# Kernel tuning notes

Measured on AMD Instinct MI355X. Metric: run time of the kernel, lower is better.

The kernel has to match this reference:

```python
import jax, jax.numpy as jnp
import numpy as np

# dims
N, T, DIN = 256, 32, 2048      # batch, time, gpt output dim
H = 2048                        # MLP hidden
G, C, D = 2, 16, 256            # vq groups, codebook size, code dim
W, A = 5, 7                     # action window, action dim
WA = W * A                      # output_size
DEC_H = 512                     # vqvae decoder hidden
NT = N * T


def _mk(key, shape, scale=0.02):
    return jax.random.normal(key, shape, dtype=jnp.float32) * scale


def setup_inputs() -> dict:
    key = jax.random.key(0)
    ks = jax.random.split(key, 16)
    inp = {
        "x": jax.random.normal(ks[0], (N, T, DIN), dtype=jnp.float32),
        # bin1 MLP: DIN -> H -> H -> C
        "w11": _mk(ks[1], (DIN, H)), "b11": jnp.zeros((H,), jnp.float32),
        "w12": _mk(ks[2], (H, H)),   "b12": jnp.zeros((H,), jnp.float32),
        "w13": _mk(ks[3], (H, C)),   "b13": jnp.zeros((C,), jnp.float32),
        # bin2 MLP: DIN+C -> H -> C
        "w21": _mk(ks[4], (DIN + C, H)), "b21": jnp.zeros((H,), jnp.float32),
        "w22": _mk(ks[5], (H, C)),       "b22": jnp.zeros((C,), jnp.float32),
        # offset MLP: DIN -> H -> H -> G*C*WA
        "wo1": _mk(ks[6], (DIN, H)), "bo1": jnp.zeros((H,), jnp.float32),
        "wo2": _mk(ks[7], (H, H)),   "bo2": jnp.zeros((H,), jnp.float32),
        "wo3": _mk(ks[8], (H, G * C * WA)), "bo3": jnp.zeros((G * C * WA,), jnp.float32),
        # residual-VQ codebooks: (G, C, D)
        "codebook": _mk(ks[9], (G, C, D), scale=1.0),
        # frozen vqvae decoder: G*D -> DEC_H -> WA
        "wd1": _mk(ks[10], (G * D, DEC_H)), "bd1": jnp.zeros((DEC_H,), jnp.float32),
        "wd2": _mk(ks[11], (DEC_H, WA)),    "bd2": jnp.zeros((WA,), jnp.float32),
    }
    return inp


def reference(x, w11, b11, w12, b12, w13, b13, w21, b21, w22, b22,
              wo1, bo1, wo2, bo2, wo3, bo3, codebook, wd1, bd1, wd2, bd2):
    xf = x.reshape(NT, DIN)
    # bin1 logits
    h = jax.nn.relu(xf @ w11 + b11)
    h = jax.nn.relu(h @ w12 + b12)
    cbet_logits1 = h @ w13 + b13                       # (NT, C)
    # offsets
    o = jax.nn.relu(xf @ wo1 + bo1)
    o = jax.nn.relu(o @ wo2 + bo2)
    cbet_offsets = (o @ wo3 + bo3).reshape(NT, G, C, WA)
    # multinomial sampling (== categorical over softmax(logits))
    key = jax.random.key(42)
    k1, k2 = jax.random.split(key)
    s1 = jax.random.categorical(k1, cbet_logits1)      # (NT,)
    one_hot1 = jax.nn.one_hot(s1, C, dtype=xf.dtype)
    h2 = jax.nn.relu(jnp.concatenate([xf, one_hot1], axis=1) @ w21 + b21)
    cbet_logits2 = h2 @ w22 + b22                      # (NT, C)
    s2 = jax.random.categorical(k2, cbet_logits2)
    sampled_centers = jnp.stack([s1, s2], axis=1)      # (NT, G)
    # gather offsets at sampled codes, sum over groups
    nt_idx = jnp.arange(NT)[:, None]
    g_idx = jnp.arange(G)[None, :]
    sampled_offsets = cbet_offsets[nt_idx, g_idx, sampled_centers].sum(axis=1)  # (NT, WA)
    # vq codebook lookup + frozen decoder (detached in torch)
    centers = codebook[g_idx, sampled_centers]          # (NT, G, D)
    dec_in = jax.lax.stop_gradient(centers.reshape(NT, G * D))
    decoded = jax.nn.relu(dec_in @ wd1 + bd1) @ wd2 + bd2
    decoded = jax.lax.stop_gradient(decoded)            # (NT, WA)
    predicted = (decoded.reshape(NT, W, A) + sampled_offsets.reshape(NT, W, A))
    predicted_action = predicted.reshape(N, T, WA)
    return predicted_action, decoded, cbet_logits1, cbet_logits2, sampled_centers
```

## Files before the change

### kernel.cpp

```cpp
#include <hip/hip_runtime.h>
#include <cstdint>
#include <cstddef>

#define NT_   8192
#define DIN_  2048
#define H_    2048
#define C_    16
#define G_    2
#define D_    256
#define WA_   35
#define DECH_ 512
#define NPAD_ 1152

typedef _Float16 f16;
typedef _Float16 h4 __attribute__((ext_vector_type(4)));
typedef _Float16 h8 __attribute__((ext_vector_type(8)));
typedef float fx4 __attribute__((ext_vector_type(4)));

typedef __attribute__((address_space(1))) const void gvoid_t;
typedef __attribute__((address_space(3))) void lvoid_t;

__device__ __forceinline__ void gld16(const void* g, void* l) {
  __builtin_amdgcn_global_load_lds((gvoid_t*)(uintptr_t)g,
                                   (lvoid_t*)(uint32_t)(uintptr_t)l, 16, 0, 0);
}

__device__ __forceinline__ void barrier_() {
  asm volatile("" ::: "memory");
  __builtin_amdgcn_s_barrier();
  asm volatile("" ::: "memory");
}

#define MFMA_(d, a, b) d = __builtin_amdgcn_mfma_f32_16x16x32_f16(a, b, d, 0, 0, 0)

__host__ __device__ inline void tf2x32(uint32_t k0, uint32_t k1,
                                       uint32_t x0, uint32_t x1,
                                       uint32_t& o0, uint32_t& o1) {
  const uint32_t ks2 = k0 ^ k1 ^ 0x1BD11BDAu;
  uint32_t ks[3] = {k0, k1, ks2};
  x0 += ks[0]; x1 += ks[1];
  const uint32_t R0[4] = {13u, 15u, 26u, 6u};
  const uint32_t R1[4] = {17u, 29u, 16u, 24u};
#pragma unroll
  for (int g = 0; g < 5; ++g) {
    const uint32_t* R = (g & 1) ? R1 : R0;
#pragma unroll
    for (int r = 0; r < 4; ++r) {
      x0 += x1;
      x1 = (x1 << R[r]) | (x1 >> (32u - R[r]));
      x1 ^= x0;
    }
    x0 += ks[(g + 1) % 3];
    x1 += ks[(g + 2) % 3] + (uint32_t)(g + 1);
  }
  o0 = x0; o1 = x1;
}

__global__ __launch_bounds__(256) void xsplit_kernel(
    const float* __restrict__ x, f16* __restrict__ xh, f16* __restrict__ xl) {
  const size_t i = (size_t)blockIdx.x * 256 + threadIdx.x;
  const float4 v0 = *(const float4*)(x + i * 8);
  const float4 v1 = *(const float4*)(x + i * 8 + 4);
  float vv[8] = {v0.x, v0.y, v0.z, v0.w, v1.x, v1.y, v1.z, v1.w};
  h8 hh, ll;
#pragma unroll
  for (int k = 0; k < 8; ++k) {
    const f16 h = (f16)vv[k];
    hh[k] = h;
    ll[k] = (f16)(vv[k] - (float)h);
  }
  *(h8*)(xh + i * 8) = hh;
  *(h8*)(xl + i * 8) = ll;
}

enum { EPI_PAIR = 0, EPI_HI = 1, EPI_LOGIT = 2 };

template <int TERMS, int GATHER, int EPI>
__global__ __launch_bounds__(512, 2) void gemm256(
    const f16* __restrict__ Ah, const f16* __restrict__ Al,
    const f16* __restrict__ Bh, const f16* __restrict__ Bl,
    const float* __restrict__ bias,
    f16* __restrict__ Chi, f16* __restrict__ Clo,
    int M, int N, int K,
    const int* __restrict__ gidx, const float* __restrict__ growp, int gldw,
    const float* __restrict__ wlog, float* __restrict__ part) {
  extern __shared__ f16 lds[];
  constexpr int BS = ((TERMS == 3) ? 4 : 2) * 8192;
  constexpr int NGLD = (TERMS == 3) ? 8 : 4;

  const int tid  = threadIdx.x;
  const int wave = tid >> 6;
  const int lane = tid & 63;
  const int lr   = lane & 15;

  const int nb  = N >> 8;
  const int nwg = (int)gridDim.x;
  const int qq  = nwg >> 3;
  const int sw  = ((int)blockIdx.x & 7) * qq + ((int)blockIdx.x >> 3);
  const int by  = sw / nb, bx = sw % nb;
  const int m0  = by << 8, n0 = bx << 8;

  const int wm = (wave >> 2) * 128;
  const int wn = (wave & 3) * 64;

  fx4 acc[8][4];
#pragma unroll
  for (int i = 0; i < 8; ++i)
#pragma unroll
    for (int j = 0; j < 4; ++j) acc[i][j] = (fx4){0.f, 0.f, 0.f, 0.f};

  const int r_row = wave * 16 + (lane >> 2);
  const int r_g   = (lane & 3) ^ ((lane >> 3) & 3);
  const f16* gsrc[NGLD];
  int gdst[NGLD];
  {
    int nr = 0;
    auto AR = [&](const f16* P, int mn, int reg, int rb) {
      gsrc[nr] = P + (size_t)(mn + rb + r_row) * K + r_g * 8;
      gdst[nr] = reg * 8192 + rb * 32 + wave * 512;
      ++nr;
    };
    if constexpr (TERMS == 3) {
      AR(Ah, m0, 0, 0); AR(Ah, m0, 0, 128);
      AR(Al, m0, 1, 0); AR(Al, m0, 1, 128);
      AR(Bh, n0, 2, 0); AR(Bh, n0, 2, 128);
      AR(Bl, n0, 3, 0); AR(Bl, n0, 3, 128);
    } else {
      AR(Ah, m0, 0, 0); AR(Ah, m0, 0, 128);
      AR(Bh, n0, 1, 0); AR(Bh, n0, 1, 128);
    }
  }

#pragma unroll
  for (int r = 0; r < NGLD; ++r) gld16(gsrc[r], lds + gdst[r]);
  asm volatile("s_waitcnt vmcnt(0)" ::: "memory");
  barrier_();

  const int pg8 = ((lane >> 4) ^ ((lr >> 1) & 3)) * 8;
  const int KT  = K >> 5;

  for (int t = 0; t < KT; ++t) {
    f16* const sb  = lds + (t & 1) * BS;
    f16* const nsb = lds + ((t + 1) & 1) * BS;
    const int ktn = (t + 1 < KT ? t + 1 : t) * 32;

    const f16* sAh = sb;
    const f16* sAl = sb + 8192;
    const f16* sBh = sb + (TERMS == 3 ? 2 : 1) * 8192;
    const f16* sBl = sb + 3 * 8192;

    h8 vbh[4], vbl[4], va[4];
#pragma unroll
    for (int j = 0; j < 4; ++j) {
      vbh[j] = *(const h8*)(sBh + (wn + j * 16 + lr) * 32 + pg8);
      if constexpr (TERMS == 3)
        vbl[j] = *(const h8*)(sBl + (wn + j * 16 + lr) * 32 + pg8);
    }
#pragma unroll
    for (int i = 0; i < 4; ++i)
      va[i] = *(const h8*)(sAh + (wm + i * 16 + lr) * 32 + pg8);
    gld16(gsrc[0] + ktn, nsb + gdst[0]);
    gld16(gsrc[1] + ktn, nsb + gdst[1]);
    if constexpr (TERMS == 3) gld16(gsrc[2] + ktn, nsb + gdst[2]);
    barrier_();
    asm volatile("s_waitcnt lgkmcnt(0)" ::: "memory");
    __builtin_amdgcn_sched_barrier(0);
    __builtin_amdgcn_s_setprio(1);
#pragma unroll
    for (int i = 0; i < 4; ++i)
#pragma unroll
      for (int j = 0; j < 4; ++j) MFMA_(acc[i][j], va[i], vbh[j]);
    if constexpr (TERMS == 3) {
#pragma unroll
      for (int i = 0; i < 4; ++i)
#pragma unroll
        for (int j = 0; j < 4; ++j) MFMA_(acc[i][j], va[i], vbl[j]);
    }
    __builtin_amdgcn_s_setprio(0);
    barrier_();
#pragma unroll
    for (int i = 0; i < 4; ++i)
      va[i] = *(const h8*)(sAh + (wm + 64 + i * 16 + lr) * 32 + pg8);
    if constexpr (TERMS == 3) {
      gld16(gsrc[3] + ktn, nsb + gdst[3]);
      gld16(gsrc[4] + ktn, nsb + gdst[4]);
      gld16(gsrc[5] + ktn, nsb + gdst[5]);
    } else {
      gld16(gsrc[2] + ktn, nsb + gdst[2]);
      gld16(gsrc[3] + ktn, nsb + gdst[3]);
    }
    barrier_();
    asm volatile("s_waitcnt lgkmcnt(0)" ::: "memory");
    __builtin_amdgcn_sched_barrier(0);
    __builtin_amdgcn_s_setprio(1);
#pragma unroll
    for (int i = 0; i < 4; ++i)
#pragma unroll
      for (int j = 0; j < 4; ++j) MFMA_(acc[4 + i][j], va[i], vbh[j]);
    if constexpr (TERMS == 3) {
#pragma unroll
      for (int i = 0; i < 4; ++i)
#pragma unroll
        for (int j = 0; j < 4; ++j) MFMA_(acc[4 + i][j], va[i], vbl[j]);
    }
    __builtin_amdgcn_s_setprio(0);
    if constexpr (TERMS != 3) asm volatile("s_waitcnt vmcnt(0)" ::: "memory");
    barrier_();
    if constexpr (TERMS == 3) {
      h8 vl0[4], vl1[4];
#pragma unroll
      for (int i = 0; i < 4; ++i) {
        vl0[i] = *(const h8*)(sAl + (wm + i * 16 + lr) * 32 + pg8);
        vl1[i] = *(const h8*)(sAl + (wm + 64 + i * 16 + lr) * 32 + pg8);
      }
      gld16(gsrc[6] + ktn, nsb + gdst[6]);
      gld16(gsrc[7] + ktn, nsb + gdst[7]);
      barrier_();
      asm volatile("s_waitcnt lgkmcnt(0)" ::: "memory");
      __builtin_amdgcn_sched_barrier(0);
      __builtin_amdgcn_s_setprio(1);
#pragma unroll
      for (int i = 0; i < 4; ++i)
#pragma unroll
        for (int j = 0; j < 4; ++j) {
          MFMA_(acc[i][j], vl0[i], vbh[j]);
          MFMA_(acc[4 + i][j], vl1[i], vbh[j]);
        }
      __builtin_amdgcn_s_setprio(0);
      asm volatile("s_waitcnt vmcnt(0)" ::: "memory");
      barrier_();
    }
  }

  const int rq = (lane >> 4) * 4;
  if constexpr (EPI == EPI_LOGIT) {
#pragma unroll
    for (int mi = 0; mi < 8; ++mi) {
#pragma unroll
      for (int q = 0; q < 4; ++q) {
        const int row = m0 + wm + mi * 16 + rq + q;
        const float* gr = nullptr;
        if constexpr (GATHER) gr = growp + (size_t)gidx[row] * gldw;
#pragma unroll
        for (int j = 0; j < 4; ++j) {
          const int col = n0 + wn + j * 16 + lr;
          float v = acc[mi][j][q] + bias[col];
          if constexpr (GATHER) v += gr[col];
          acc[mi][j][q] = fmaxf(v, 0.f);
        }
      }
    }
    const int sidx = bx * 4 + (wave & 3);
    float* pout = part + ((size_t)sidx * NT_ + (m0 + wm)) * 16;
    const int qw = lr >> 2, cw = lr & 3;
#pragma unroll
    for (int cc = 0; cc < 4; ++cc) {
      float4 wv[4];
#pragma unroll
      for (int j = 0; j < 4; ++j)
        wv[j] = *(const float4*)(wlog + (size_t)(n0 + wn + j * 16 + lr) * 16 + cc * 4);
#pragma unroll
      for (int mi = 0; mi < 8; ++mi) {
        float pl[4][4] = {{0.f}};
#pragma unroll
        for (int j = 0; j < 4; ++j)
#pragma unroll
          for (int q = 0; q < 4; ++q) {
            pl[q][0] += acc[mi][j][q] * wv[j].x;
            pl[q][1] += acc[mi][j][q] * wv[j].y;
            pl[q][2] += acc[mi][j][q] * wv[j].z;
            pl[q][3] += acc[mi][j][q] * wv[j].w;
          }
#pragma unroll
        for (int st = 1; st < 16; st <<= 1) {
#pragma unroll
          for (int q = 0; q < 4; ++q)
#pragma unroll
            for (int c = 0; c < 4; ++c) pl[q][c] += __shfl_xor(pl[q][c], st);
        }
        pout[(size_t)(mi * 16 + rq + qw) * 16 + cc * 4 + cw] = pl[qw][cw];
      }
    }
  } else {
#pragma unroll
    for (int mi = 0; mi < 8; ++mi) {
#pragma unroll
      for (int q = 0; q < 4; ++q) {
        const int row = m0 + wm + mi * 16 + rq + q;
#pragma unroll
        for (int j = 0; j < 4; ++j) {
          const int col = n0 + wn + j * 16 + lr;
          float v = fmaxf(acc[mi][j][q] + bias[col], 0.f);
          const f16 hh = (f16)v;
          Chi[(size_t)row * N + col] = hh;
          if constexpr (EPI == EPI_PAIR)
            Clo[(size_t)row * N + col] = (f16)(v - (float)hh);
        }
      }
    }
  }
}

template <int RELU>
__global__ __launch_bounds__(256, 2) void gemm128(
    const f16* __restrict__ Ah, const f16* __restrict__ Bh,
    const float* __restrict__ bias, f16* __restrict__ Chi,
    int M, int N, int K) {
  __shared__ f16 lds[2 * 4096];
  f16* sAh = lds;
  f16* sBh = lds + 4096;

  const int tid  = threadIdx.x;
  const int wave = tid >> 6;
  const int lane = tid & 63;
  const int n0 = blockIdx.x * 128;
  const int m0 = blockIdx.y * 128;
  const int wm = (wave >> 1) * 64;
  const int wn = (wave & 1) * 64;
  const int lr = lane & 15;
  const int lk = (lane >> 4) * 8;

  fx4 acc[4][4];
#pragma unroll
  for (int i = 0; i < 4; ++i)
#pragma unroll
    for (int j = 0; j < 4; ++j) acc[i][j] = (fx4){0.f, 0.f, 0.f, 0.f};

  const int sb = wave * 2048 + (lane << 4);

  for (int kt = 0; kt < K; kt += 32) {
#pragma unroll
    for (int c = 0; c < 2; ++c) {
      const int boff = sb + c * 1024;
      const int row  = boff >> 6;
      const int col  = (boff & 63) >> 1;
      gld16(Bh + (size_t)(n0 + row) * K + kt + col, sBh + (wave * 2 + c) * 512);
      gld16(Ah + (size_t)(m0 + row) * K + kt + col, sAh + (wave * 2 + c) * 512);
    }
    __syncthreads();

    h8 ah[4], bh[4];
#pragma unroll
    for (int t = 0; t < 4; ++t) {
      ah[t] = *(const h8*)&sAh[(wm + t * 16 + lr) * 32 + lk];
      bh[t] = *(const h8*)&sBh[(wn + t * 16 + lr) * 32 + lk];
    }
#pragma unroll
    for (int i = 0; i < 4; ++i)
#pragma unroll
      for (int j = 0; j < 4; ++j) MFMA_(acc[i][j], ah[i], bh[j]);
    __syncthreads();
  }

  const int rq = (lane >> 4) * 4;
#pragma unroll
  for (int i = 0; i < 4; ++i) {
#pragma unroll
    for (int q = 0; q < 4; ++q) {
      const int row = m0 + wm + i * 16 + rq + q;
#pragma unroll
      for (int j = 0; j < 4; ++j) {
        const int col = n0 + wn + j * 16 + lr;
        float v = acc[i][j][q];
        if (bias) v += bias[col];
        if constexpr (RELU) v = fmaxf(v, 0.f);
        Chi[(size_t)row * N + col] = (f16)v;
      }
    }
  }
}

template <int SPLIT>
__global__ __launch_bounds__(256) void wtransT(
    const float* __restrict__ src, f16* __restrict__ hi, f16* __restrict__ lo,
    int K, int N, int Npad) {
  __shared__ float t[32][33];
  const int bn = blockIdx.x * 32;
  const int bk = blockIdx.y * 32;
  const int tx = threadIdx.x & 31, ty = threadIdx.x >> 5;
#pragma unroll
  for (int r = ty; r < 32; r += 8) {
    const float v = (bn + tx < N) ? src[(size_t)(bk + r) * N + bn + tx] : 0.f;
    t[tx][r] = v;
  }
  __syncthreads();
#pragma unroll
  for (int r = ty; r < 32; r += 8) {
    const float v = t[r][tx];
    const f16 hh = (f16)v;
    hi[(size_t)(bn + r) * K + bk + tx] = hh;
    if (SPLIT) lo[(size_t)(bn + r) * K + bk + tx] = (f16)(v - (float)hh);
  }
}

__global__ __launch_bounds__(256) void reduce_sample(
    const float* __restrict__ part, const float* __restrict__ bias,
    float* __restrict__ logits_out, int* __restrict__ s_out,
    float* __restrict__ centers_out, uint32_t ka, uint32_t kb, int which) {
  const int tid = threadIdx.x;
  const int c = tid & 15;
  const int m = blockIdx.x * 16 + (tid >> 4);
  float v = bias[c];
#pragma unroll 8
  for (int s = 0; s < 32; ++s) v += part[((size_t)s * NT_ + m) * 16 + c];
  logits_out[(size_t)m * C_ + c] = v;
  const uint32_t j = (uint32_t)(m * C_ + c);
  uint32_t o0, o1;
  tf2x32(ka, kb, 0u, j, o0, o1);
  const uint32_t bits = o0 ^ o1;
  float u = __uint_as_float((bits >> 9) | 0x3f800000u) - 1.0f;
  u = fmaxf(1.17549435e-38f, u);
  float z = -logf(-logf(u)) + v;
  int bi = c;
#pragma unroll
  for (int st = 1; st < 16; st <<= 1) {
    const float oz = __shfl_xor(z, st);
    const int   ob = __shfl_xor(bi, st);
    if (oz > z || (oz == z && ob < bi)) { z = oz; bi = ob; }
  }
  if (c == 0) {
    s_out[m] = bi;
    centers_out[(size_t)m * G_ + which] = (float)bi;
  }
}

__global__ void gather_dec_kernel(const float* __restrict__ codebook,
                                  const int* __restrict__ s1,
                                  const int* __restrict__ s2,
                                  f16* __restrict__ dec_in) {
  const int idx = blockIdx.x * blockDim.x + threadIdx.x;
  const int m = idx >> 9, d = idx & 511;
  const int g = d >> 8, dd = d & 255;
  const int s = g ? s2[m] : s1[m];
  dec_in[idx] = (f16)codebook[(size_t)(g * C_ + s) * D_ + dd];
}

__global__ __launch_bounds__(320) void final2(
    const f16* __restrict__ P,
    const float* __restrict__ bo3,
    const f16* __restrict__ dech,
    const float* __restrict__ wd2, const float* __restrict__ bd2,
    const int* __restrict__ s1, const int* __restrict__ s2,
    float* __restrict__ out_pred, float* __restrict__ out_dec) {
  __shared__ float drow[DECH_];
  const int m = blockIdx.x;
  for (int i = threadIdx.x; i < DECH_; i += 320)
    drow[i] = (float)dech[(size_t)m * DECH_ + i];
  __syncthreads();
  const int a1 = s1[m], a2 = s2[m];
  const int c = threadIdx.x >> 3, g = threadIdx.x & 7;
  float pdec = 0.f;
  if (c < WA_) {
    for (int i = 0; i < DECH_ / 8; ++i) {
      const int k = g * (DECH_ / 8) + i;
      pdec = fmaf(drow[k], wd2[(size_t)k * WA_ + c], pdec);
    }
  }
#pragma unroll
  for (int off = 1; off < 8; off <<= 1) pdec += __shfl_xor(pdec, off);
  if (c < WA_ && g == 0) {
    const float dec = pdec + bd2[c];
    const float soff = (float)P[(size_t)m * NPAD_ + a1 * WA_ + c]
                     + (float)P[(size_t)m * NPAD_ + C_ * WA_ + a2 * WA_ + c]
                     + bo3[a1 * WA_ + c] + bo3[C_ * WA_ + a2 * WA_ + c];
    out_dec[(size_t)m * WA_ + c] = dec;
    out_pred[(size_t)m * WA_ + c] = dec + soff;
  }
}

extern "C" void kernel_launch(void* const* d_in, const int* in_sizes, int n_in,
                              void* d_out, int out_size, void* d_ws, size_t ws_size,
                              hipStream_t stream) {
  const float* x    = (const float*)d_in[0];
  const float* w11  = (const float*)d_in[1];
  const float* b11  = (const float*)d_in[2];
  const float* w12  = (const float*)d_in[3];
  const float* b12  = (const float*)d_in[4];
  const float* w13  = (const float*)d_in[5];
  const float* b13  = (const float*)d_in[6];
  const float* w21  = (const float*)d_in[7];
  const float* b21  = (const float*)d_in[8];
  const float* w22  = (const float*)d_in[9];
  const float* b22  = (const float*)d_in[10];
  const float* wo1  = (const float*)d_in[11];
  const float* bo1  = (const float*)d_in[12];
  const float* wo2  = (const float*)d_in[13];
  const float* bo2  = (const float*)d_in[14];
  const float* wo3  = (const float*)d_in[15];
  const float* bo3  = (const float*)d_in[16];
  const float* cbk  = (const float*)d_in[17];
  const float* wd1  = (const float*)d_in[18];
  const float* bd1  = (const float*)d_in[19];
  const float* wd2  = (const float*)d_in[20];
  const float* bd2  = (const float*)d_in[21];

  float* out = (float*)d_out;
  float* out_pred = out;
  float* out_dec  = out + (size_t)NT_ * WA_;
  float* out_l1   = out + (size_t)2 * NT_ * WA_;
  float* out_l2   = out_l1 + (size_t)NT_ * C_;
  float* out_sc   = out_l2 + (size_t)NT_ * C_;

  const size_t AB = (size_t)NT_ * H_;
  f16*   Xh   = (f16*)d_ws;
  f16*   Xl   = Xh + AB;
  f16*   H1a  = Xl + AB;
  f16*   H1b  = H1a + AB;
  f16*   WH   = H1b + AB;
  f16*   WL   = WH + (size_t)H_ * H_;
  float* PART = (float*)(WL + (size_t)H_ * H_);
  int*   S1   = (int*)(PART + (size_t)32 * NT_ * C_);
  int*   S2   = S1 + NT_;

  f16* O1    = H1a;
  f16* O2    = H1b;
  f16* P     = Xh;
  f16* DECIN = Xl;
  f16* DECH  = Xl + (size_t)NT_ * DECH_;

  hipFuncSetAttribute(reinterpret_cast<const void*>(&gemm256<3,0,EPI_PAIR>),
                      hipFuncAttributeMaxDynamicSharedMemorySize, 131072);
  hipFuncSetAttribute(reinterpret_cast<const void*>(&gemm256<3,0,EPI_LOGIT>),
                      hipFuncAttributeMaxDynamicSharedMemorySize, 131072);
  hipFuncSetAttribute(reinterpret_cast<const void*>(&gemm256<3,1,EPI_LOGIT>),
                      hipFuncAttributeMaxDynamicSharedMemorySize, 131072);
  hipFuncSetAttribute(reinterpret_cast<const void*>(&gemm256<1,0,EPI_HI>),
                      hipFuncAttributeMaxDynamicSharedMemorySize, 65536);

  uint32_t k1a, k1b, k2a, k2b;
  tf2x32(0u, 42u, 0u, 0u, k1a, k1b);
  tf2x32(0u, 42u, 0u, 1u, k2a, k2b);

  const dim3 b256(256), b512(512);
  const dim3 gW(H_ / 32, H_ / 32);
  const dim3 gWo3(NPAD_ / 32, H_ / 32);
  const dim3 gWd1(DECH_ / 32, DECH_ / 32);
  const dim3 gBig((NT_ / 256) * (H_ / 256));
  const dim3 gP(NPAD_ / 128, NT_ / 128);
  const dim3 gD(DECH_ / 128, NT_ / 128);

  xsplit_kernel<<<NT_ * H_ / (8 * 256), b256, 0, stream>>>(x, Xh, Xl);

  wtransT<1><<<gW, b256, 0, stream>>>(w11, WH, WL, H_, H_, H_);
  gemm256<3,0,EPI_PAIR><<<gBig, b512, 131072, stream>>>(
      Xh, Xl, WH, WL, b11, H1a, H1b, NT_, H_, DIN_,
      nullptr, nullptr, 0, nullptr, nullptr);
  wtransT<1><<<gW, b256, 0, stream>>>(w12, WH, WL, H_, H_, H_);
  gemm256<3,0,EPI_LOGIT><<<gBig, b512, 131072, stream>>>(
      H1a, H1b, WH, WL, b12, nullptr, nullptr, NT_, H_, H_,
      nullptr, nullptr, 0, w13, PART);
  reduce_sample<<<NT_ / 16, b256, 0, stream>>>(PART, b13, out_l1, S1, out_sc,
                                               k1a, k1b, 0);

  wtransT<1><<<gW, b256, 0, stream>>>(w21, WH, WL, H_, H_, H_);
  gemm256<3,1,EPI_LOGIT><<<gBig, b512, 131072, stream>>>(
      Xh, Xl, WH, WL, b21, nullptr, nullptr, NT_, H_, DIN_,
      S1, w21 + (size_t)DIN_ * H_, H_, w22, PART);
  reduce_sample<<<NT_ / 16, b256, 0, stream>>>(PART, b22, out_l2, S2, out_sc,
                                               k2a, k2b, 1);

  wtransT<0><<<gW, b256, 0, stream>>>(wo1, WH, nullptr, H_, H_, H_);
  gemm256<1,0,EPI_HI><<<gBig, b512, 65536, stream>>>(
      Xh, nullptr, WH, nullptr, bo1, O1, nullptr, NT_, H_, DIN_,
      nullptr, nullptr, 0, nullptr, nullptr);
  wtransT<0><<<gW, b256, 0, stream>>>(wo2, WH, nullptr, H_, H_, H_);
  gemm256<1,0,EPI_HI><<<gBig, b512, 65536, stream>>>(
      O1, nullptr, WH, nullptr, bo2, O2, nullptr, NT_, H_, H_,
      nullptr, nullptr, 0, nullptr, nullptr);
  wtransT<0><<<gWo3, b256, 0, stream>>>(wo3, WH, nullptr, H_, G_ * C_ * WA_, NPAD_);
  gemm128<0><<<gP, b256, 0, stream>>>(O2, WH, nullptr, P, NT_, NPAD_, H_);

  gather_dec_kernel<<<(NT_ * DECH_) / 256, b256, 0, stream>>>(cbk, S1, S2, DECIN);
  wtransT<0><<<gWd1, b256, 0, stream>>>(wd1, WH, nullptr, DECH_, DECH_, DECH_);
  gemm128<1><<<gD, b256, 0, stream>>>(DECIN, WH, bd1, DECH, NT_, DECH_, DECH_);

  final2<<<NT_, 320, 0, stream>>>(P, bo3, DECH, wd2, bd2, S1, S2,
                                  out_pred, out_dec);

  (void)in_sizes; (void)n_in; (void)out_size; (void)ws_size;
}
```

Baseline: 1.064 ms.

## Add triple-buffered single-term GEMM and relax vmcnt waits in split GEMM

```diff
diff --git a/kernel.cpp b/kernel.cpp
--- a/kernel.cpp
+++ b/kernel.cpp
@@ -31,6 +31,14 @@
   asm volatile("" ::: "memory");
 }
 
+template <int N>
+__device__ __forceinline__ void waitvm() {
+  if constexpr (N == 8)      asm volatile("s_waitcnt vmcnt(8)" ::: "memory");
+  else if constexpr (N == 6) asm volatile("s_waitcnt vmcnt(6)" ::: "memory");
+  else if constexpr (N == 2) asm volatile("s_waitcnt vmcnt(2)" ::: "memory");
+  else                       asm volatile("s_waitcnt vmcnt(0)" ::: "memory");
+}
+
 #define MFMA_(d, a, b) d = __builtin_amdgcn_mfma_f32_16x16x32_f16(a, b, d, 0, 0, 0)
 
 __host__ __device__ inline void tf2x32(uint32_t k0, uint32_t k1,
@@ -75,7 +83,7 @@
 
 enum { EPI_PAIR = 0, EPI_HI = 1, EPI_LOGIT = 2 };
 
-template <int TERMS, int GATHER, int EPI>
+template <int GATHER, int EPI>
 __global__ __launch_bounds__(512, 2) void gemm256(
     const f16* __restrict__ Ah, const f16* __restrict__ Al,
     const f16* __restrict__ Bh, const f16* __restrict__ Bl,
@@ -85,8 +93,7 @@
     const int* __restrict__ gidx, const float* __restrict__ growp, int gldw,
     const float* __restrict__ wlog, float* __restrict__ part) {
   extern __shared__ f16 lds[];
-  constexpr int BS = ((TERMS == 3) ? 4 : 2) * 8192;
-  constexpr int NGLD = (TERMS == 3) ? 8 : 4;
+  constexpr int BS = 4 * 8192;
 
   const int tid  = threadIdx.x;
   const int wave = tid >> 6;
@@ -111,8 +118,8 @@
 
   const int r_row = wave * 16 + (lane >> 2);
   const int r_g   = (lane & 3) ^ ((lane >> 3) & 3);
-  const f16* gsrc[NGLD];
-  int gdst[NGLD];
+  const f16* gsrc[8];
+  int gdst[8];
   {
     int nr = 0;
     auto AR = [&](const f16* P, int mn, int reg, int rb) {
@@ -120,20 +127,15 @@
       gdst[nr] = reg * 8192 + rb * 32 + wave * 512;
       ++nr;
     };
-    if constexpr (TERMS == 3) {
-      AR(Ah, m0, 0, 0); AR(Ah, m0, 0, 128);
-      AR(Al, m0, 1, 0); AR(Al, m0, 1, 128);
-      AR(Bh, n0, 2, 0); AR(Bh, n0, 2, 128);
-      AR(Bl, n0, 3, 0); AR(Bl, n0, 3, 128);
-    } else {
-      AR(Ah, m0, 0, 0); AR(Ah, m0, 0, 128);
-      AR(Bh, n0, 1, 0); AR(Bh, n0, 1, 128);
-    }
-  }
-
-#pragma unroll
-  for (int r = 0; r < NGLD; ++r) gld16(gsrc[r], lds + gdst[r]);
-  asm volatile("s_waitcnt vmcnt(0)" ::: "memory");
+    AR(Bh, n0, 2, 0); AR(Bh, n0, 2, 128);
+    AR(Bl, n0, 3, 0); AR(Bl, n0, 3, 128);
+    AR(Ah, m0, 0, 0); AR(Ah, m0, 0, 128);
+    AR(Al, m0, 1, 0); AR(Al, m0, 1, 128);
+  }
+
+#pragma unroll
+  for (int r = 0; r < 8; ++r) gld16(gsrc[r], lds + gdst[r]);
+  waitvm<2>();
   barrier_();
 
   const int pg8 = ((lane >> 4) ^ ((lr >> 1) & 3)) * 8;
@@ -146,22 +148,21 @@
 
     const f16* sAh = sb;
     const f16* sAl = sb + 8192;
-    const f16* sBh = sb + (TERMS == 3 ? 2 : 1) * 8192;
-    const f16* sBl = sb + 3 * 8192;
+    const f16* sBh = sb + 16384;
+    const f16* sBl = sb + 24576;
 
     h8 vbh[4], vbl[4], va[4];
 #pragma unroll
     for (int j = 0; j < 4; ++j) {
       vbh[j] = *(const h8*)(sBh + (wn + j * 16 + lr) * 32 + pg8);
-      if constexpr (TERMS == 3)
-        vbl[j] = *(const h8*)(sBl + (wn + j * 16 + lr) * 32 + pg8);
+      vbl[j] = *(const h8*)(sBl + (wn + j * 16 + lr) * 32 + pg8);
     }
 #pragma unroll
     for (int i = 0; i < 4; ++i)
       va[i] = *(const h8*)(sAh + (wm + i * 16 + lr) * 32 + pg8);
     gld16(gsrc[0] + ktn, nsb + gdst[0]);
     gld16(gsrc[1] + ktn, nsb + gdst[1]);
-    if constexpr (TERMS == 3) gld16(gsrc[2] + ktn, nsb + gdst[2]);
+    gld16(gsrc[2] + ktn, nsb + gdst[2]);
     barrier_();
     asm volatile("s_waitcnt lgkmcnt(0)" ::: "memory");
     __builtin_amdgcn_sched_barrier(0);
@@ -170,25 +171,18 @@
     for (int i = 0; i < 4; ++i)
 #pragma unroll
       for (int j = 0; j < 4; ++j) MFMA_(acc[i][j], va[i], vbh[j]);
-    if constexpr (TERMS == 3) {
-#pragma unroll
-      for (int i = 0; i < 4; ++i)
-#pragma unroll
-        for (int j = 0; j < 4; ++j) MFMA_(acc[i][j], va[i], vbl[j]);
-    }
+#pragma unroll
+    for (int i = 0; i < 4; ++i)
+#pragma unroll
+      for (int j = 0; j < 4; ++j) MFMA_(acc[i][j], va[i], vbl[j]);
     __builtin_amdgcn_s_setprio(0);
     barrier_();
 #pragma unroll
     for (int i = 0; i < 4; ++i)
       va[i] = *(const h8*)(sAh + (wm + 64 + i * 16 + lr) * 32 + pg8);
-    if constexpr (TERMS == 3) {
-      gld16(gsrc[3] + ktn, nsb + gdst[3]);
-      gld16(gsrc[4] + ktn, nsb + gdst[4]);
-      gld16(gsrc[5] + ktn, nsb + gdst[5]);
-    } else {
-      gld16(gsrc[2] + ktn, nsb + gdst[2]);
-      gld16(gsrc[3] + ktn, nsb + gdst[3]);
-    }
+    gld16(gsrc[3] + ktn, nsb + gdst[3]);
+    gld16(gsrc[4] + ktn, nsb + gdst[4]);
+    gld16(gsrc[5] + ktn, nsb + gdst[5]);
     barrier_();
     asm volatile("s_waitcnt lgkmcnt(0)" ::: "memory");
     __builtin_amdgcn_sched_barrier(0);
@@ -197,16 +191,14 @@
     for (int i = 0; i < 4; ++i)
 #pragma unroll
       for (int j = 0; j < 4; ++j) MFMA_(acc[4 + i][j], va[i], vbh[j]);
-    if constexpr (TERMS == 3) {
-#pragma unroll
-      for (int i = 0; i < 4; ++i)
-#pragma unroll
-        for (int j = 0; j < 4; ++j) MFMA_(acc[4 + i][j], va[i], vbl[j]);
-    }
+#pragma unroll
+    for (int i = 0; i < 4; ++i)
+#pragma unroll
+      for (int j = 0; j < 4; ++j) MFMA_(acc[4 + i][j], va[i], vbl[j]);
     __builtin_amdgcn_s_setprio(0);
-    if constexpr (TERMS != 3) asm volatile("s_waitcnt vmcnt(0)" ::: "memory");
+    waitvm<6>();
     barrier_();
-    if constexpr (TERMS == 3) {
+    {
       h8 vl0[4], vl1[4];
 #pragma unroll
       for (int i = 0; i < 4; ++i) {
@@ -227,7 +219,7 @@
           MFMA_(acc[4 + i][j], vl1[i], vbh[j]);
         }
       __builtin_amdgcn_s_setprio(0);
-      asm volatile("s_waitcnt vmcnt(0)" ::: "memory");
+      waitvm<2>();
       barrier_();
     }
   }
@@ -250,36 +242,58 @@
         }
       }
     }
+    waitvm<0>();
+    barrier_();
+    float* psm = (float*)lds + wave * 2560;
     const int sidx = bx * 4 + (wave & 3);
-    float* pout = part + ((size_t)sidx * NT_ + (m0 + wm)) * 16;
-    const int qw = lr >> 2, cw = lr & 3;
+    const int q_l = ((lr & 1) << 1) | ((lr >> 1) & 1);
+    const int c_l = (((lr >> 2) & 1) << 1) | ((lr >> 3) & 1);
 #pragma unroll
     for (int cc = 0; cc < 4; ++cc) {
-      float4 wv[4];
-#pragma unroll
-      for (int j = 0; j < 4; ++j)
-        wv[j] = *(const float4*)(wlog + (size_t)(n0 + wn + j * 16 + lr) * 16 + cc * 4);
+      float wc[4][4];
+#pragma unroll
+      for (int j = 0; j < 4; ++j) {
+        const float4 wv = *(const float4*)(wlog +
+            (size_t)(n0 + wn + j * 16 + lr) * 16 + cc * 4);
+        wc[j][0] = wv.x; wc[j][1] = wv.y; wc[j][2] = wv.z; wc[j][3] = wv.w;
+      }
 #pragma unroll
       for (int mi = 0; mi < 8; ++mi) {
-        float pl[4][4] = {{0.f}};
-#pragma unroll
-        for (int j = 0; j < 4; ++j)
-#pragma unroll
-          for (int q = 0; q < 4; ++q) {
-            pl[q][0] += acc[mi][j][q] * wv[j].x;
-            pl[q][1] += acc[mi][j][q] * wv[j].y;
-            pl[q][2] += acc[mi][j][q] * wv[j].z;
-            pl[q][3] += acc[mi][j][q] * wv[j].w;
+        float A[16];
+#pragma unroll
+        for (int i = 0; i < 16; ++i) {
+          float s = 0.f;
+#pragma unroll
+          for (int j = 0; j < 4; ++j)
+            s = fmaf(acc[mi][j][i >> 2], wc[j][i & 3], s);
+          A[i] = s;
+        }
+#pragma unroll
+        for (int k = 0; k < 4; ++k) {
+          const int L2 = 8 >> k;
+          const bool b = (lr >> k) & 1;
+          float An[8];
+#pragma unroll
+          for (int i = 0; i < L2; ++i) {
+            const float keep = b ? A[i + L2] : A[i];
+            const float send = b ? A[i] : A[i + L2];
+            An[i] = keep + __shfl_xor(send, 1 << k);
           }
 #pragma unroll
-        for (int st = 1; st < 16; st <<= 1) {
-#pragma unroll
-          for (int q = 0; q < 4; ++q)
-#pragma unroll
-            for (int c = 0; c < 4; ++c) pl[q][c] += __shfl_xor(pl[q][c], st);
+          for (int i = 0; i < L2; ++i) A[i] = An[i];
         }
-        pout[(size_t)(mi * 16 + rq + qw) * 16 + cc * 4 + cw] = pl[qw][cw];
-      }
+        psm[mi * 320 + (rq + q_l) * 20 + cc * 4 + c_l] = A[0];
+      }
+    }
+    asm volatile("s_waitcnt lgkmcnt(0)" ::: "memory");
+#pragma unroll
+    for (int mi = 0; mi < 8; ++mi) {
+      const float4 o = *(const float4*)(psm + mi * 320 +
+                                        (lane >> 2) * 20 + (lane & 3) * 4);
+      float* pout = part + ((size_t)sidx * NT_ +
+                            (m0 + wm + mi * 16 + (lane >> 2))) * 16 +
+                    (lane & 3) * 4;
+      *(float4*)pout = o;
     }
   } else {
 #pragma unroll
@@ -296,6 +310,107 @@
           if constexpr (EPI == EPI_PAIR)
             Clo[(size_t)row * N + col] = (f16)(v - (float)hh);
         }
+      }
+    }
+  }
+}
+
+__global__ __launch_bounds__(512, 2) void gemm256_1t(
+    const f16* __restrict__ Ah, const f16* __restrict__ Bh,
+    const float* __restrict__ bias, f16* __restrict__ Chi,
+    int M, int N, int K) {
+  extern __shared__ f16 lds[];
+  constexpr int BS = 16384;
+
+  const int tid  = threadIdx.x;
+  const int wave = tid >> 6;
+  const int lane = tid & 63;
+  const int lr   = lane & 15;
+
+  const int nb  = N >> 8;
+  const int nwg = (int)gridDim.x;
+  const int qq  = nwg >> 3;
+  const int sw  = ((int)blockIdx.x & 7) * qq + ((int)blockIdx.x >> 3);
+  const int by  = sw / nb, bx = sw % nb;
+  const int m0  = by << 8, n0 = bx << 8;
+
+  const int wm = (wave >> 2) * 128;
+  const int wn = (wave & 3) * 64;
+
+  fx4 acc[8][4];
+#pragma unroll
+  for (int i = 0; i < 8; ++i)
+#pragma unroll
+    for (int j = 0; j < 4; ++j) acc[i][j] = (fx4){0.f, 0.f, 0.f, 0.f};
+
+  const int r_row = wave * 16 + (lane >> 2);
+  const int r_g   = (lane & 3) ^ ((lane >> 3) & 3);
+  const f16* gsrc[4];
+  int gdst[4];
+  {
+    int nr = 0;
+    auto AR = [&](const f16* P, int mn, int reg, int rb) {
+      gsrc[nr] = P + (size_t)(mn + rb + r_row) * K + r_g * 8;
+      gdst[nr] = reg * 8192 + rb * 32 + wave * 512;
+      ++nr;
+    };
+    AR(Ah, m0, 0, 0); AR(Ah, m0, 0, 128);
+    AR(Bh, n0, 1, 0); AR(Bh, n0, 1, 128);
+  }
+
+  const int KT  = K >> 5;
+  const int pg8 = ((lane >> 4) ^ ((lr >> 1) & 3)) * 8;
+
+#pragma unroll
+  for (int r = 0; r < 4; ++r) gld16(gsrc[r], lds + gdst[r]);
+#pragma unroll
+  for (int r = 0; r < 4; ++r) gld16(gsrc[r] + 32, lds + BS + gdst[r]);
+
+  int cur = 0, nn = 2;
+  for (int t = 0; t < KT; ++t) {
+    const int ktn = (t + 2 < KT ? t + 2 : KT - 1) * 32;
+    f16* const nsb = lds + nn * BS;
+#pragma unroll
+    for (int r = 0; r < 4; ++r) gld16(gsrc[r] + ktn, nsb + gdst[r]);
+    waitvm<8>();
+    barrier_();
+
+    const f16* sb = lds + cur * BS;
+    h8 vb[4], va0[4], va1[4];
+#pragma unroll
+    for (int j = 0; j < 4; ++j)
+      vb[j] = *(const h8*)(sb + 8192 + (wn + j * 16 + lr) * 32 + pg8);
+#pragma unroll
+    for (int i = 0; i < 4; ++i) {
+      va0[i] = *(const h8*)(sb + (wm + i * 16 + lr) * 32 + pg8);
+      va1[i] = *(const h8*)(sb + (wm + 64 + i * 16 + lr) * 32 + pg8);
+    }
+    asm volatile("s_waitcnt lgkmcnt(0)" ::: "memory");
+    __builtin_amdgcn_sched_barrier(0);
+    __builtin_amdgcn_s_setprio(1);
+#pragma unroll
+    for (int i = 0; i < 4; ++i)
+#pragma unroll
+      for (int j = 0; j < 4; ++j) {
+        MFMA_(acc[i][j], va0[i], vb[j]);
+        MFMA_(acc[4 + i][j], va1[i], vb[j]);
+      }
+    __builtin_amdgcn_s_setprio(0);
+    barrier_();
+    cur = (cur == 2) ? 0 : cur + 1;
+    nn  = (nn == 2) ? 0 : nn + 1;
+  }
+
+  const int rq = (lane >> 4) * 4;
+#pragma unroll
+  for (int mi = 0; mi < 8; ++mi) {
+#pragma unroll
+    for (int q = 0; q < 4; ++q) {
+      const int row = m0 + wm + mi * 16 + rq + q;
+#pragma unroll
+      for (int j = 0; j < 4; ++j) {
+        const int col = n0 + wn + j * 16 + lr;
+        Chi[(size_t)row * N + col] = (f16)fmaxf(acc[mi][j][q] + bias[col], 0.f);
       }
     }
   }
@@ -518,14 +633,14 @@
   f16* DECIN = Xl;
   f16* DECH  = Xl + (size_t)NT_ * DECH_;
 
-  hipFuncSetAttribute(reinterpret_cast<const void*>(&gemm256<3,0,EPI_PAIR>),
+  hipFuncSetAttribute(reinterpret_cast<const void*>(&gemm256<0,EPI_PAIR>),
                       hipFuncAttributeMaxDynamicSharedMemorySize, 131072);
-  hipFuncSetAttribute(reinterpret_cast<const void*>(&gemm256<3,0,EPI_LOGIT>),
+  hipFuncSetAttribute(reinterpret_cast<const void*>(&gemm256<0,EPI_LOGIT>),
                       hipFuncAttributeMaxDynamicSharedMemorySize, 131072);
-  hipFuncSetAttribute(reinterpret_cast<const void*>(&gemm256<3,1,EPI_LOGIT>),
+  hipFuncSetAttribute(reinterpret_cast<const void*>(&gemm256<1,EPI_LOGIT>),
                       hipFuncAttributeMaxDynamicSharedMemorySize, 131072);
-  hipFuncSetAttribute(reinterpret_cast<const void*>(&gemm256<1,0,EPI_HI>),
-                      hipFuncAttributeMaxDynamicSharedMemorySize, 65536);
+  hipFuncSetAttribute(reinterpret_cast<const void*>(&gemm256_1t),
+                      hipFuncAttributeMaxDynamicSharedMemorySize, 98304);
 
   uint32_t k1a, k1b, k2a, k2b;
   tf2x32(0u, 42u, 0u, 0u, k1a, k1b);
@@ -542,31 +657,27 @@
   xsplit_kernel<<<NT_ * H_ / (8 * 256), b256, 0, stream>>>(x, Xh, Xl);
 
   wtransT<1><<<gW, b256, 0, stream>>>(w11, WH, WL, H_, H_, H_);
-  gemm256<3,0,EPI_PAIR><<<gBig, b512, 131072, stream>>>(
+  gemm256<0,EPI_PAIR><<<gBig, b512, 131072, stream>>>(
       Xh, Xl, WH, WL, b11, H1a, H1b, NT_, H_, DIN_,
       nullptr, nullptr, 0, nullptr, nullptr);
   wtransT<1><<<gW, b256, 0, stream>>>(w12, WH, WL, H_, H_, H_);
-  gemm256<3,0,EPI_LOGIT><<<gBig, b512, 131072, stream>>>(
+  gemm256<0,EPI_LOGIT><<<gBig, b512, 131072, stream>>>(
       H1a, H1b, WH, WL, b12, nullptr, nullptr, NT_, H_, H_,
       nullptr, nullptr, 0, w13, PART);
   reduce_sample<<<NT_ / 16, b256, 0, stream>>>(PART, b13, out_l1, S1, out_sc,
                                                k1a, k1b, 0);
 
   wtransT<1><<<gW, b256, 0, stream>>>(w21, WH, WL, H_, H_, H_);
-  gemm256<3,1,EPI_LOGIT><<<gBig, b512, 131072, stream>>>(
+  gemm256<1,EPI_LOGIT><<<gBig, b512, 131072, stream>>>(
       Xh, Xl, WH, WL, b21, nullptr, nullptr, NT_, H_, DIN_,
       S1, w21 + (size_t)DIN_ * H_, H_, w22, PART);
   reduce_sample<<<NT_ / 16, b256, 0, stream>>>(PART, b22, out_l2, S2, out_sc,
                                                k2a, k2b, 1);
 
   wtransT<0><<<gW, b256, 0, stream>>>(wo1, WH, nullptr, H_, H_, H_);
-  gemm256<1,0,EPI_HI><<<gBig, b512, 65536, stream>>>(
-      Xh, nullptr, WH, nullptr, bo1, O1, nullptr, NT_, H_, DIN_,
-      nullptr, nullptr, 0, nullptr, nullptr);
+  gemm256_1t<<<gBig, b512, 98304, stream>>>(Xh, WH, bo1, O1, NT_, H_, DIN_);
   wtransT<0><<<gW, b256, 0, stream>>>(wo2, WH, nullptr, H_, H_, H_);
-  gemm256<1,0,EPI_HI><<<gBig, b512, 65536, stream>>>(
-      O1, nullptr, WH, nullptr, bo2, O2, nullptr, NT_, H_, H_,
-      nullptr, nullptr, 0, nullptr, nullptr);
+  gemm256_1t<<<gBig, b512, 98304, stream>>>(O1, WH, bo2, O2, NT_, H_, H_);
   wtransT<0><<<gWo3, b256, 0, stream>>>(wo3, WH, nullptr, H_, G_ * C_ * WA_, NPAD_);
   gemm128<0><<<gP, b256, 0, stream>>>(O2, WH, nullptr, P, NT_, NPAD_, H_);
 
```

After: 950.2 us. 10.7% less time.
